# Optimization experiments

Measured on AMD Instinct MI355X. Metric: run time of the kernel, lower is better.

## Reference

```python
import jax, jax.numpy as jnp
import numpy as np

POLY_DEGREE = 2
EPS = 1e-10
MAX_INTER = 25

# Upper-triangle index pairs (i<j) in the same row-major order as the
# original double loop: (0,1),(0,2),...,(0,24),(1,2),...
_IU0, _IU1 = np.triu_indices(MAX_INTER, k=1)


def setup_inputs() -> dict:
    key = jax.random.key(0)
    x = jax.random.normal(key, (524288, 25), dtype=jnp.float32)
    return {"x": x}


def reference(x) -> jnp.ndarray:
    feats = [x]
    # polynomial features: degrees 2..POLY_DEGREE
    for degree in range(2, POLY_DEGREE + 1):
        feats.append(jnp.power(x, degree))
    ax = jnp.abs(x) + EPS
    feats.append(jnp.log(ax))            # log features
    feats.append(jnp.sqrt(ax))           # sqrt features
    feats.append(jnp.power(ax, 1.0 / 3.0))  # cbrt features
    # pairwise interactions among first min(F,25) columns, upper triangle
    inter = x[:, _IU0] * x[:, _IU1]      # [B, 300]
    feats.append(inter)
    return jnp.concatenate(feats, axis=1)  # [B, 400]
```

## Files before the change

### kernel.cpp

```cpp
#include <hip/hip_runtime.h>

#define NF    25
#define NPAIR 300
#define NCOL  425
#define ROWS  8
#define BLK   256
#define TILE4 (ROWS * NCOL / 4)
#define NP_TOT (ROWS * NPAIR)
#define KFULL  (NP_TOT / BLK)
#define KREM   (NP_TOT - KFULL * BLK)

typedef float f32x4 __attribute__((ext_vector_type(4)));
typedef unsigned int u32;

__global__ __launch_bounds__(BLK) void feat_expand_kernel(
    const float* __restrict__ x, float* __restrict__ out,
    int nrows, int nchunks) {
  __shared__ f32x4 tile4[TILE4];
  __shared__ float xs[ROWS * NF];
  float* tile = (float*)tile4;

  const int tid = threadIdx.x;
  const int r200 = tid / NF, i200 = tid - r200 * NF;

  u32 ab[KFULL + 1];
  u32 ti[KFULL + 1];
#pragma unroll
  for (int k = 0; k <= KFULL; ++k) {
    int p = tid + k * BLK;
    if (p >= NP_TOT) p = 0;
    const int r = p / NPAIR;
    const int q = p - r * NPAIR;
    int rem = q, i = 0;
    while (rem >= (NF - 1 - i)) { rem -= (NF - 1 - i); ++i; }
    const int j = i + 1 + rem;
    ab[k] = (u32)(r * NF + i) | ((u32)(r * NF + j) << 16);
    ti[k] = (u32)(r * NCOL + 5 * NF + q);
  }

  for (int chunk = blockIdx.x; chunk < nchunks; chunk += gridDim.x) {
    const long long rowbase = (long long)chunk * ROWS;
    const long long remr = nrows - rowbase;
    const int rows_here = (int)(remr < ROWS ? remr : ROWS);

    float v = 0.0f;
    if (tid < ROWS * NF) {
      if (r200 < rows_here) v = x[rowbase * NF + tid];
      xs[tid] = v;
    }
    __syncthreads();

    if (tid < ROWS * NF) {
      float* tr = &tile[r200 * NCOL];
      const float ax = fabsf(v) + 1e-10f;
      const float l2 = __builtin_amdgcn_logf(ax);
      tr[i200]        = v;
      tr[NF + i200]   = v * v;
      tr[2*NF + i200] = l2 * 0.69314718055994530942f;
      tr[3*NF + i200] = sqrtf(ax);
      tr[4*NF + i200] = __builtin_amdgcn_exp2f(l2 * (1.0f/3.0f));
    }

#pragma unroll
    for (int k = 0; k <= KFULL; ++k) {
      if (k < KFULL || tid < KREM) {
        const u32 d = ab[k];
        tile[ti[k]] = xs[d & 0xFFFF] * xs[d >> 16];
      }
    }
    __syncthreads();

    if (rows_here == ROWS) {
      f32x4* __restrict__ o4 = (f32x4*)(out + rowbase * NCOL);
#pragma unroll
      for (int k = 0; k < 4; ++k) {
        const int v4 = tid + k * BLK;
        if (k < 3 || v4 < TILE4)
          __builtin_nontemporal_store(tile4[v4], &o4[v4]);
      }
    } else {
      const int total = rows_here * NCOL;
      for (int o = tid; o < total; o += BLK)
        out[rowbase * NCOL + o] = tile[o];
    }
  }
}

extern "C" void kernel_launch(void* const* d_in, const int* in_sizes, int n_in,
                              void* d_out, int out_size, void* d_ws, size_t ws_size,
                              hipStream_t stream) {
  const float* x = (const float*)d_in[0];
  float* out = (float*)d_out;

  const int nrows = in_sizes[0] / NF;
  const int nchunks = (nrows + ROWS - 1) / ROWS;
  const int grid = nchunks < 4096 ? nchunks : 4096;

  feat_expand_kernel<<<grid, BLK, 0, stream>>>(x, out, nrows, nchunks);
}
```

Before: 208.5 us.

## Double-buffer LDS tile and input to overlap compute with stores

Adds two LDS buffers for the output tile and the staged inputs, and software-pipelines the grid-stride loop. While one tile is being stored, the next chunk is computed and the chunk after that is loaded, which cuts the loop to one barrier per chunk. This is meant to hide global load latency and store issue behind compute. It roughly doubles LDS use per block, which may lower occupancy.

```diff
diff --git a/kernel.cpp b/kernel.cpp
--- a/kernel.cpp
+++ b/kernel.cpp
@@ -5,7 +5,7 @@
 #define NCOL  425
 #define ROWS  8
 #define BLK   256
-#define TILE4 (ROWS * NCOL / 4)
+#define TILE4N 850
 #define NP_TOT (ROWS * NPAIR)
 #define KFULL  (NP_TOT / BLK)
 #define KREM   (NP_TOT - KFULL * BLK)
@@ -16,9 +16,8 @@
 __global__ __launch_bounds__(BLK) void feat_expand_kernel(
     const float* __restrict__ x, float* __restrict__ out,
     int nrows, int nchunks) {
-  __shared__ f32x4 tile4[TILE4];
-  __shared__ float xs[ROWS * NF];
-  float* tile = (float*)tile4;
+  __shared__ f32x4 tile4[2][TILE4N];
+  __shared__ float xs[2][ROWS * NF];
 
   const int tid = threadIdx.x;
   const int r200 = tid / NF, i200 = tid - r200 * NF;
@@ -33,24 +32,25 @@
     const int q = p - r * NPAIR;
     int rem = q, i = 0;
     while (rem >= (NF - 1 - i)) { rem -= (NF - 1 - i); ++i; }
-    const int j = i + 1 + rem;
-    ab[k] = (u32)(r * NF + i) | ((u32)(r * NF + j) << 16);
+    ab[k] = (u32)(r * NF + i) | ((u32)(r * NF + i + 1 + rem) << 16);
     ti[k] = (u32)(r * NCOL + 5 * NF + q);
   }
 
-  for (int chunk = blockIdx.x; chunk < nchunks; chunk += gridDim.x) {
-    const long long rowbase = (long long)chunk * ROWS;
-    const long long remr = nrows - rowbase;
-    const int rows_here = (int)(remr < ROWS ? remr : ROWS);
+  const long long G  = gridDim.x;
+  const long long c0 = blockIdx.x;
 
-    float v = 0.0f;
+  auto stageA = [&](int b, long long cc) {
     if (tid < ROWS * NF) {
-      if (r200 < rows_here) v = x[rowbase * NF + tid];
-      xs[tid] = v;
+      const long long rowbase = cc * ROWS;
+      float v = 0.0f;
+      if (rowbase + r200 < nrows) v = x[rowbase * NF + tid];
+      xs[b][tid] = v;
     }
-    __syncthreads();
-
+  };
+  auto stageB = [&](int bt, int bx) {
+    float* tile = (float*)tile4[bt];
     if (tid < ROWS * NF) {
+      const float v = xs[bx][tid];
       float* tr = &tile[r200 * NCOL];
       const float ax = fabsf(v) + 1e-10f;
       const float l2 = __builtin_amdgcn_logf(ax);
@@ -60,29 +60,44 @@
       tr[3*NF + i200] = sqrtf(ax);
       tr[4*NF + i200] = __builtin_amdgcn_exp2f(l2 * (1.0f/3.0f));
     }
-
 #pragma unroll
     for (int k = 0; k <= KFULL; ++k) {
       if (k < KFULL || tid < KREM) {
         const u32 d = ab[k];
-        tile[ti[k]] = xs[d & 0xFFFF] * xs[d >> 16];
+        tile[ti[k]] = xs[bx][d & 0xFFFF] * xs[bx][d >> 16];
       }
     }
-    __syncthreads();
+  };
 
+  if (c0 < nchunks) stageA(0, c0);
+  __syncthreads();
+  if (c0 < nchunks) stageB(0, 0);
+  if (c0 + G < nchunks) stageA(1, c0 + G);
+  __syncthreads();
+
+  int par = 0;
+  for (long long chunk = c0; chunk < nchunks; chunk += G, par ^= 1) {
+    const long long rowbase = chunk * ROWS;
+    const long long remr = nrows - rowbase;
+    const int rows_here = (int)(remr < ROWS ? remr : ROWS);
     if (rows_here == ROWS) {
       f32x4* __restrict__ o4 = (f32x4*)(out + rowbase * NCOL);
 #pragma unroll
       for (int k = 0; k < 4; ++k) {
         const int v4 = tid + k * BLK;
-        if (k < 3 || v4 < TILE4)
-          __builtin_nontemporal_store(tile4[v4], &o4[v4]);
+        if (k < 3 || v4 < TILE4N)
+          __builtin_nontemporal_store(tile4[par][v4], &o4[v4]);
       }
     } else {
+      const float* tile = (const float*)tile4[par];
       const int total = rows_here * NCOL;
       for (int o = tid; o < total; o += BLK)
         out[rowbase * NCOL + o] = tile[o];
     }
+
+    if (chunk + G < nchunks)     stageB(par ^ 1, par ^ 1);
+    if (chunk + 2*G < nchunks)   stageA(par, chunk + 2*G);
+    __syncthreads();
   }
 }
 
```

Result: no change. 206.0 us (-1.2%).
